# Kernel tuning notes

Hardware: AMD Instinct MI355X
Metric: run time of the kernel (lower is better)

The kernel has to match this reference:

```python
import jax, jax.numpy as jnp
import numpy as np

B, S, E = 4, 2048, 1024
H, D, F = 16, 64, 4096
EPS = 1e-5


def layer_norm(x, gamma, beta):
    mu = jnp.mean(x, axis=-1, keepdims=True)
    var = jnp.mean(jnp.square(x - mu), axis=-1, keepdims=True)
    return (x - mu) * jax.lax.rsqrt(var + EPS) * gamma + beta


def setup_inputs() -> dict:
    key = jax.random.key(0)
    ks = jax.random.split(key, 8)
    scale = 0.02  # keep logits in a numerically sane range
    X = jax.random.normal(ks[0], (B, S, E), dtype=jnp.float32)
    WQ = jax.random.normal(ks[1], (H, E, D), dtype=jnp.float32) * scale
    WK = jax.random.normal(ks[2], (H, E, D), dtype=jnp.float32) * scale
    WV = jax.random.normal(ks[3], (H, E, D), dtype=jnp.float32) * scale
    WO = jax.random.normal(ks[4], (H * D, E), dtype=jnp.float32) * scale
    gamma = jnp.ones((E,), dtype=jnp.float32)
    beta = jnp.zeros((E,), dtype=jnp.float32)
    W1 = jax.random.normal(ks[5], (E, F), dtype=jnp.float32) * scale
    b1 = jnp.zeros((F,), dtype=jnp.float32)
    W2 = jax.random.normal(ks[6], (F, E), dtype=jnp.float32) * scale
    b2 = jnp.zeros((E,), dtype=jnp.float32)
    return {"X": X, "WQ": WQ, "WK": WK, "WV": WV, "WO": WO,
            "gamma": gamma, "beta": beta, "W1": W1, "b1": b1, "W2": W2, "b2": b2}


def reference(X, WQ, WK, WV, WO, gamma, beta, W1, b1, W2, b2):
    # Batched-over-heads version of the per-head python loop (same math).
    Q = jnp.einsum('bse,hed->bhsd', X, WQ)  # [B,H,S,D]
    K = jnp.einsum('bse,hed->bhsd', X, WK)
    V = jnp.einsum('bse,hed->bhsd', X, WV)
    scores = jnp.einsum('bhsd,bhtd->bhst', Q, K)  # [B,H,S,T]
    # FAITHFUL quirk: torch.softmax(..., dim=1) on a [B,S,S] tensor normalizes
    # over the QUERY axis (axis=2 here), then divides by sqrt(D) AFTER softmax.
    att = jax.nn.softmax(scores, axis=2) / jnp.sqrt(jnp.float32(D))
    vec = jnp.einsum('bhst,bhtd->bhsd', att, V)  # [B,H,S,D]
    att_vec = jnp.transpose(vec, (0, 2, 1, 3)).reshape(X.shape[0], X.shape[1], H * D)
    vector_att = layer_norm(att_vec @ WO + X, gamma, beta)
    vector_ffn = jax.nn.relu(vector_att @ W1 + b1) @ W2 + b2
    return layer_norm(vector_ffn + vector_att, gamma, beta)
```

## Files before the change

### kernel.cpp

```cpp
#include <hip/hip_runtime.h>
#include <cstddef>
#include <cstdint>

#define BB 4
#define SS 2048
#define EE 1024
#define HH 16
#define DD 64
#define FF 4096

typedef unsigned short u16;
typedef __attribute__((ext_vector_type(8))) short short8;
typedef __attribute__((ext_vector_type(4))) short short4v;
typedef __attribute__((ext_vector_type(4))) float f32x4;

__device__ __forceinline__ u16 f2bf(float x) {
    unsigned u = __builtin_bit_cast(unsigned, x);
    u += 0x7fffu + ((u >> 16) & 1u);
    return (u16)(u >> 16);
}
__device__ __forceinline__ float bf2f(u16 h) {
    unsigned u = ((unsigned)h) << 16;
    return __builtin_bit_cast(float, u);
}

#define GLD_LDS16(g, l)                                                     \
    __builtin_amdgcn_global_load_lds(                                       \
        (const __attribute__((address_space(1))) void*)(g),                 \
        (__attribute__((address_space(3))) void*)(l), 16, 0, 0)

__global__ __launch_bounds__(256) void cvt_bf(const float* __restrict__ in,
                                              u16* __restrict__ out, int n4) {
    const int i = blockIdx.x * 256 + threadIdx.x;
    if (i < n4) {
        float4 v = reinterpret_cast<const float4*>(in)[i];
        short4v o;
        o.x = (short)f2bf(v.x); o.y = (short)f2bf(v.y);
        o.z = (short)f2bf(v.z); o.w = (short)f2bf(v.w);
        reinterpret_cast<short4v*>(out)[i] = o;
    }
}

__global__ __launch_bounds__(256) void transp_bf(const float* __restrict__ in,
                                                 u16* __restrict__ out, int R, int C) {
    __shared__ float T[64][65];
    const int r0 = blockIdx.x * 64, c0 = blockIdx.y * 64;
    const size_t zoff = (size_t)blockIdx.z * R * C;
    in += zoff; out += zoff;
    const int tid = threadIdx.x;
#pragma unroll 4
    for (int i = 0; i < 16; ++i) {
        int l = tid + i * 256;
        T[l >> 6][l & 63] = in[(size_t)(r0 + (l >> 6)) * C + c0 + (l & 63)];
    }
    __syncthreads();
#pragma unroll 4
    for (int i = 0; i < 16; ++i) {
        int l = tid + i * 256;
        out[(size_t)(c0 + (l >> 6)) * R + r0 + (l & 63)] = f2bf(T[l & 63][l >> 6]);
    }
}

template <int EPI>
__global__ __launch_bounds__(256) void gemm_bf16(const u16* __restrict__ A,
                                                 const u16* __restrict__ BT,
                                                 int K, int N,
                                                 void* __restrict__ Cout,
                                                 const float* __restrict__ bias,
                                                 const void* __restrict__ resid) {
    __shared__ u16 As[128 * 32];
    __shared__ u16 Bs[128 * 32];
    const int tid = threadIdx.x;
    const int w = tid >> 6, l = tid & 63;
    const int quad = l >> 4, lane16 = l & 15;
    const int wr = (w >> 1) * 64, wc = (w & 1) * 64;
    const int m0 = blockIdx.x * 128, n0 = blockIdx.y * 128;
    const int drow = w * 32 + (l >> 2);
    const int dk = (l & 3) * 8;
    const u16* Ag = A + (size_t)(m0 + drow) * K + dk;
    const u16* Bg = BT + (size_t)(n0 + drow) * K + dk;
    const size_t r16 = (size_t)16 * K;
    u16* AsD = &As[w * 1024];
    u16* BsD = &Bs[w * 1024];

    f32x4 acc[4][4] = {};
    for (int k0 = 0; k0 < K; k0 += 32) {
        __syncthreads();
        GLD_LDS16(Ag + k0, AsD);
        GLD_LDS16(Ag + k0 + r16, AsD + 512);
        GLD_LDS16(Bg + k0, BsD);
        GLD_LDS16(Bg + k0 + r16, BsD + 512);
        __syncthreads();
        short8 af[4], bf[4];
#pragma unroll
        for (int mf = 0; mf < 4; ++mf)
            af[mf] = *(const short8*)&As[(wr + mf * 16 + lane16) * 32 + quad * 8];
#pragma unroll
        for (int nf = 0; nf < 4; ++nf)
            bf[nf] = *(const short8*)&Bs[(wc + nf * 16 + lane16) * 32 + quad * 8];
#pragma unroll
        for (int mf = 0; mf < 4; ++mf)
#pragma unroll
            for (int nf = 0; nf < 4; ++nf)
                acc[mf][nf] = __builtin_amdgcn_mfma_f32_16x16x32_bf16(af[mf], bf[nf], acc[mf][nf], 0, 0, 0);
    }

#pragma unroll
    for (int mf = 0; mf < 4; ++mf) {
        const int row = m0 + wr + mf * 16 + quad * 4;
#pragma unroll
        for (int nf = 0; nf < 4; ++nf) {
            const int col = n0 + wc + nf * 16 + lane16;
#pragma unroll
            for (int r = 0; r < 4; ++r) {
                float v = acc[mf][nf][r];
                const size_t idx = (size_t)(row + r) * N + col;
                if (EPI == 0) {
                    ((u16*)Cout)[idx] = f2bf(v);
                } else if (EPI == 1) {
                    ((float*)Cout)[idx] = v + ((const float*)resid)[idx];
                } else if (EPI == 2) {
                    v += bias[col];
                    ((u16*)Cout)[idx] = f2bf(fmaxf(v, 0.f));
                } else {
                    v += bias[col] + bf2f(((const u16*)resid)[idx]);
                    ((float*)Cout)[idx] = v;
                }
            }
        }
    }
}

__global__ __launch_bounds__(256) void stats_l(const u16* __restrict__ Qg,
                                               const u16* __restrict__ Kg,
                                               float* __restrict__ Ls) {
    __shared__ u16 Qt[64 * 72];
    const int t0 = blockIdx.x * 128;
    const int bh = blockIdx.y;
    const int b = bh >> 4, h = bh & 15;
    const int tid = threadIdx.x;
    const int w = tid >> 6, l = tid & 63;
    const int quad = l >> 4, lane16 = l & 15;
    const u16* Qp = Qg + (size_t)b * SS * 1024 + h * 64;
    const u16* Kp = Kg + (size_t)b * SS * 1024 + h * 64;
    const int sr = tid >> 3;
    const int dg = (tid & 7) * 8;

    short8 kf[2][2];
#pragma unroll
    for (int nf = 0; nf < 2; ++nf)
#pragma unroll
        for (int ks = 0; ks < 2; ++ks)
            kf[nf][ks] = *(const short8*)(Kp +
                (size_t)(t0 + w * 32 + nf * 16 + lane16) * 1024 + ks * 32 + quad * 8);

    const u16* qsrc0 = Qp + (size_t)sr * 1024 + dg;
    short8 pq0 = *(const short8*)qsrc0;
    short8 pq1 = *(const short8*)(qsrc0 + (size_t)32 * 1024);

    float lcol[2] = {0.f, 0.f};
    for (int st = 0; st < 32; ++st) {
        __syncthreads();
        *(short8*)&Qt[sr * 72 + dg] = pq0;
        *(short8*)&Qt[(sr + 32) * 72 + dg] = pq1;
        __syncthreads();
        if (st + 1 < 32) {
            const u16* qsrc = Qp + (size_t)((st + 1) * 64 + sr) * 1024 + dg;
            pq0 = *(const short8*)qsrc;
            pq1 = *(const short8*)(qsrc + (size_t)32 * 1024);
        }
        f32x4 sc[4][2] = {};
#pragma unroll
        for (int ks = 0; ks < 2; ++ks) {
#pragma unroll
            for (int mf = 0; mf < 4; ++mf) {
                short8 afr = *(const short8*)&Qt[(mf * 16 + lane16) * 72 + ks * 32 + quad * 8];
#pragma unroll
                for (int nf = 0; nf < 2; ++nf)
                    sc[mf][nf] = __builtin_amdgcn_mfma_f32_16x16x32_bf16(afr, kf[nf][ks], sc[mf][nf], 0, 0, 0);
            }
        }
#pragma unroll
        for (int nf = 0; nf < 2; ++nf)
#pragma unroll
            for (int mf = 0; mf < 4; ++mf)
#pragma unroll
                for (int r = 0; r < 4; ++r) lcol[nf] += __expf(sc[mf][nf][r]);
    }
#pragma unroll
    for (int nf = 0; nf < 2; ++nf) {
        lcol[nf] += __shfl_xor(lcol[nf], 32);
        lcol[nf] += __shfl_xor(lcol[nf], 16);
        if (quad == 0)
            Ls[(size_t)bh * SS + t0 + w * 32 + nf * 16 + lane16] = lcol[nf];
    }
}

__global__ __launch_bounds__(256) void vscale(u16* __restrict__ Vtg,
                                              const float* __restrict__ Ls) {
    const int r = blockIdx.x;
    const int b = blockIdx.y;
    const int h = r >> 6;
    const int t0 = threadIdx.x * 8;
    u16* vp = Vtg + (size_t)r * 8192 + b * SS + t0;
    const float* lp = Ls + (size_t)(b * 16 + h) * SS + t0;
    short8 v = *(short8*)vp;
    short8 o;
#pragma unroll
    for (int i = 0; i < 8; ++i)
        o[i] = (short)f2bf(bf2f((u16)v[i]) * (0.125f / lp[i]));
    *(short8*)vp = o;
}

__global__ __launch_bounds__(256) void pv_fused(const u16* __restrict__ Qg,
                                                const u16* __restrict__ Kg,
                                                const u16* __restrict__ Vtg,
                                                u16* __restrict__ vecbf) {
    __shared__ u16 Ks[64 * 72];
    __shared__ u16 Vs[64 * 72];
    __shared__ u16 Ps[128 * 72];
    const int s0 = blockIdx.x * 128;
    const int bh = blockIdx.y;
    const int b = bh >> 4, h = bh & 15;
    const int tid = threadIdx.x;
    const int w = tid >> 6, l = tid & 63;
    const int quad = l >> 4, lane16 = l & 15;
    const u16* Qp = Qg + (size_t)b * SS * 1024 + h * 64;
    const u16* Kp = Kg + (size_t)b * SS * 1024 + h * 64;
    const u16* Vp = Vtg + (size_t)h * 64 * 8192 + (size_t)b * SS;
    const int sr = tid >> 3, dg = (tid & 7) * 8;

    short8 qf[2][2];
#pragma unroll
    for (int nf = 0; nf < 2; ++nf)
#pragma unroll
        for (int ks = 0; ks < 2; ++ks)
            qf[nf][ks] = *(const short8*)(Qp +
                (size_t)(s0 + w * 32 + nf * 16 + lane16) * 1024 + ks * 32 + quad * 8);

    short8 pk0 = *(const short8*)(Kp + (size_t)sr * 1024 + dg);
    short8 pk1 = *(const short8*)(Kp + (size_t)(sr + 32) * 1024 + dg);
    short8 pv0 = *(const short8*)(Vp + (size_t)sr * 8192 + dg);
    short8 pv1 = *(const short8*)(Vp + (size_t)(sr + 32) * 8192 + dg);

    f32x4 acc[2][4] = {};
    for (int tt = 0; tt < 32; ++tt) {
        __syncthreads();
        *(short8*)&Ks[sr * 72 + dg] = pk0;
        *(short8*)&Ks[(sr + 32) * 72 + dg] = pk1;
        *(short8*)&Vs[sr * 72 + dg] = pv0;
        *(short8*)&Vs[(sr + 32) * 72 + dg] = pv1;
        __syncthreads();
        if (tt + 1 < 32) {
            const int t1 = (tt + 1) * 64;
            pk0 = *(const short8*)(Kp + (size_t)(t1 + sr) * 1024 + dg);
            pk1 = *(const short8*)(Kp + (size_t)(t1 + sr + 32) * 1024 + dg);
            pv0 = *(const short8*)(Vp + (size_t)sr * 8192 + t1 + dg);
            pv1 = *(const short8*)(Vp + (size_t)(sr + 32) * 8192 + t1 + dg);
        }
        f32x4 sc[4][2] = {};
#pragma unroll
        for (int ks = 0; ks < 2; ++ks) {
#pragma unroll
            for (int mf = 0; mf < 4; ++mf) {
                short8 afr = *(const short8*)&Ks[(mf * 16 + lane16) * 72 + ks * 32 + quad * 8];
#pragma unroll
                for (int nf = 0; nf < 2; ++nf)
                    sc[mf][nf] = __builtin_amdgcn_mfma_f32_16x16x32_bf16(afr, qf[nf][ks], sc[mf][nf], 0, 0, 0);
            }
        }
#pragma unroll
        for (int mf = 0; mf < 4; ++mf)
#pragma unroll
            for (int nf = 0; nf < 2; ++nf) {
                const int srow = w * 32 + nf * 16 + lane16;
                short4v pk;
                pk.x = (short)f2bf(__expf(sc[mf][nf][0]));
                pk.y = (short)f2bf(__expf(sc[mf][nf][1]));
                pk.z = (short)f2bf(__expf(sc[mf][nf][2]));
                pk.w = (short)f2bf(__expf(sc[mf][nf][3]));
                *(short4v*)&Ps[srow * 72 + mf * 16 + quad * 4] = pk;
            }
#pragma unroll
        for (int ks = 0; ks < 2; ++ks) {
            short8 bfr[4];
#pragma unroll
            for (int nf = 0; nf < 4; ++nf)
                bfr[nf] = *(const short8*)&Vs[(nf * 16 + lane16) * 72 + ks * 32 + quad * 8];
            short8 afr[2];
#pragma unroll
            for (int mf = 0; mf < 2; ++mf)
                afr[mf] = *(const short8*)&Ps[(w * 32 + mf * 16 + lane16) * 72 + ks * 32 + quad * 8];
#pragma unroll
            for (int mf = 0; mf < 2; ++mf)
#pragma unroll
                for (int nf = 0; nf < 4; ++nf)
                    acc[mf][nf] = __builtin_amdgcn_mfma_f32_16x16x32_bf16(afr[mf], bfr[nf], acc[mf][nf], 0, 0, 0);
        }
    }
#pragma unroll
    for (int mf = 0; mf < 2; ++mf)
#pragma unroll
        for (int nf = 0; nf < 4; ++nf) {
            const int col = h * 64 + nf * 16 + lane16;
#pragma unroll
            for (int r = 0; r < 4; ++r) {
                const int srow = s0 + w * 32 + mf * 16 + quad * 4 + r;
                vecbf[(size_t)(b * SS + srow) * 1024 + col] = f2bf(acc[mf][nf][r]);
            }
        }
}

__global__ __launch_bounds__(256) void ln_bf_kernel(const float* __restrict__ buf,
                                                    const float* __restrict__ g,
                                                    const float* __restrict__ be,
                                                    u16* __restrict__ outbf) {
    const int row = blockIdx.x;
    const int tid = threadIdx.x;
    const float* p = buf + (size_t)row * EE;
    float4 x = reinterpret_cast<const float4*>(p)[tid];
    float s = x.x + x.y + x.z + x.w;
    __shared__ float red[4];
#pragma unroll
    for (int o = 32; o > 0; o >>= 1) s += __shfl_down(s, o);
    const int wid = tid >> 6, lane = tid & 63;
    if (lane == 0) red[wid] = s;
    __syncthreads();
    const float mu = (red[0] + red[1] + red[2] + red[3]) * (1.0f / EE);
    __syncthreads();
    const float dx = x.x - mu, dy = x.y - mu, dz = x.z - mu, dw = x.w - mu;
    float v = dx * dx + dy * dy + dz * dz + dw * dw;
#pragma unroll
    for (int o = 32; o > 0; o >>= 1) v += __shfl_down(v, o);
    if (lane == 0) red[wid] = v;
    __syncthreads();
    const float var = (red[0] + red[1] + red[2] + red[3]) * (1.0f / EE);
    const float rs = rsqrtf(var + 1e-5f);
    float4 gv = reinterpret_cast<const float4*>(g)[tid];
    float4 bv = reinterpret_cast<const float4*>(be)[tid];
    short4v o;
    o.x = (short)f2bf(dx * rs * gv.x + bv.x);
    o.y = (short)f2bf(dy * rs * gv.y + bv.y);
    o.z = (short)f2bf(dz * rs * gv.z + bv.z);
    o.w = (short)f2bf(dw * rs * gv.w + bv.w);
    reinterpret_cast<short4v*>(outbf + (size_t)row * EE)[tid] = o;
}

__global__ __launch_bounds__(256) void ln_kernel(float* __restrict__ buf,
                                                 const float* __restrict__ g,
                                                 const float* __restrict__ be) {
    const int row = blockIdx.x;
    const int tid = threadIdx.x;
    float* p = buf + (size_t)row * EE;
    float4 x = reinterpret_cast<float4*>(p)[tid];
    float s = x.x + x.y + x.z + x.w;
    __shared__ float red[4];
#pragma unroll
    for (int o = 32; o > 0; o >>= 1) s += __shfl_down(s, o);
    const int wid = tid >> 6, lane = tid & 63;
    if (lane == 0) red[wid] = s;
    __syncthreads();
    const float mu = (red[0] + red[1] + red[2] + red[3]) * (1.0f / EE);
    __syncthreads();
    const float dx = x.x - mu, dy = x.y - mu, dz = x.z - mu, dw = x.w - mu;
    float v = dx * dx + dy * dy + dz * dz + dw * dw;
#pragma unroll
    for (int o = 32; o > 0; o >>= 1) v += __shfl_down(v, o);
    if (lane == 0) red[wid] = v;
    __syncthreads();
    const float var = (red[0] + red[1] + red[2] + red[3]) * (1.0f / EE);
    const float rs = rsqrtf(var + 1e-5f);
    float4 gv = reinterpret_cast<const float4*>(g)[tid];
    float4 bv = reinterpret_cast<const float4*>(be)[tid];
    float4 y;
    y.x = dx * rs * gv.x + bv.x;
    y.y = dy * rs * gv.y + bv.y;
    y.z = dz * rs * gv.z + bv.z;
    y.w = dw * rs * gv.w + bv.w;
    reinterpret_cast<float4*>(p)[tid] = y;
}

extern "C" void kernel_launch(void* const* d_in, const int* in_sizes, int n_in,
                              void* d_out, int out_size, void* d_ws, size_t ws_size,
                              hipStream_t stream) {
    const float* X     = (const float*)d_in[0];
    const float* WQ    = (const float*)d_in[1];
    const float* WK    = (const float*)d_in[2];
    const float* WV    = (const float*)d_in[3];
    const float* WO    = (const float*)d_in[4];
    const float* gamma = (const float*)d_in[5];
    const float* beta  = (const float*)d_in[6];
    const float* W1    = (const float*)d_in[7];
    const float* b1    = (const float*)d_in[8];
    const float* W2    = (const float*)d_in[9];
    const float* b2    = (const float*)d_in[10];
    float* out = (float*)d_out;

    char* ws = (char*)d_ws;
    const size_t MB = 1024 * 1024;
    u16* WQT   = (u16*)(ws + 0);
    u16* WKT   = (u16*)(ws + 2 * MB);
    u16* WVT   = (u16*)(ws + 4 * MB);
    u16* WOT   = (u16*)(ws + 6 * MB);
    u16* W1T   = (u16*)(ws + 8 * MB);
    u16* W2T   = (u16*)(ws + 16 * MB);
    float* Ls  = (float*)(ws + 24 * MB);
    u16* Qbf   = (u16*)(ws + 25 * MB);
    u16* Kbf   = (u16*)(ws + 41 * MB);
    u16* Vt    = (u16*)(ws + 57 * MB);
    u16* vecbf = (u16*)(ws + 73 * MB);
    u16* hid   = (u16*)(ws + 25 * MB);
    u16* Xbf   = (u16*)(ws + 89 * MB);
    float* vatt  = (float*)(ws + 105 * MB);
    u16*   ln1bf = (u16*)(ws + 137 * MB);

    const int NT = BB * SS;

    cvt_bf<<<8192, 256, 0, stream>>>(X, Xbf, NT * EE / 4);
    transp_bf<<<dim3(16, 1, 16), 256, 0, stream>>>(WQ, WQT, EE, DD);
    transp_bf<<<dim3(16, 1, 16), 256, 0, stream>>>(WK, WKT, EE, DD);
    transp_bf<<<dim3(16, 1, 16), 256, 0, stream>>>(WV, WVT, EE, DD);
    transp_bf<<<dim3(16, 16, 1), 256, 0, stream>>>(WO, WOT, HH * DD, EE);
    transp_bf<<<dim3(16, 64, 1), 256, 0, stream>>>(W1, W1T, EE, FF);
    transp_bf<<<dim3(64, 16, 1), 256, 0, stream>>>(W2, W2T, FF, EE);

    gemm_bf16<0><<<dim3(64, 8), 256, 0, stream>>>(Xbf, WQT, EE, 1024, Qbf, nullptr, nullptr);
    gemm_bf16<0><<<dim3(64, 8), 256, 0, stream>>>(Xbf, WKT, EE, 1024, Kbf, nullptr, nullptr);
    gemm_bf16<0><<<dim3(8, 64), 256, 0, stream>>>(WVT, Xbf, EE, 8192, Vt, nullptr, nullptr);

    stats_l<<<dim3(SS / 128, BB * HH), 256, 0, stream>>>(Qbf, Kbf, Ls);
    vscale<<<dim3(1024, BB), 256, 0, stream>>>(Vt, Ls);
    pv_fused<<<dim3(SS / 128, BB * HH), 256, 0, stream>>>(Qbf, Kbf, Vt, vecbf);

    gemm_bf16<1><<<dim3(64, 8), 256, 0, stream>>>(vecbf, WOT, EE, 1024, vatt, nullptr, X);
    ln_bf_kernel<<<NT, 256, 0, stream>>>(vatt, gamma, beta, ln1bf);

    gemm_bf16<2><<<dim3(64, 32), 256, 0, stream>>>(ln1bf, W1T, EE, FF, hid, b1, nullptr);
    gemm_bf16<3><<<dim3(64, 8), 256, 0, stream>>>(hid, W2T, FF, 1024, out, b2, ln1bf);

    ln_kernel<<<NT, 256, 0, stream>>>(out, gamma, beta);
}
```

Baseline: 644.5 us.

## Keep P in registers with 32x32 MFMA and permlane swap in pv_fused

Rewrites the attention PV kernel to use 32x32x16 bf16 MFMAs so the exponentiated score tile can be repacked in registers with v_permlane32_swap instead of going through an LDS P buffer. K/V tiles switch to an XOR-swizzled unpadded LDS layout. Q is pre-scaled by log2(e) in the projection GEMM epilogue so raw v_exp_f32 (exp2) replaces __expf in both the stats and PV kernels. This removes LDS round-trips and a barrier-free store/load of P, at the cost of inline asm and a layout change that must stay consistent with the MFMA output mapping.

```diff
diff --git a/kernel.cpp b/kernel.cpp
--- a/kernel.cpp
+++ b/kernel.cpp
@@ -13,6 +13,8 @@
 typedef __attribute__((ext_vector_type(8))) short short8;
 typedef __attribute__((ext_vector_type(4))) short short4v;
 typedef __attribute__((ext_vector_type(4))) float f32x4;
+typedef __attribute__((ext_vector_type(16))) float f32x16;
+typedef __attribute__((ext_vector_type(4))) unsigned u32x4;
 
 __device__ __forceinline__ u16 f2bf(float x) {
     unsigned u = __builtin_bit_cast(unsigned, x);
@@ -22,6 +24,22 @@
 __device__ __forceinline__ float bf2f(u16 h) {
     unsigned u = ((unsigned)h) << 16;
     return __builtin_bit_cast(float, u);
+}
+__device__ __forceinline__ float ex2(float x) {
+    float r;
+    asm("v_exp_f32 %0, %1" : "=v"(r) : "v"(x));
+    return r;
+}
+__device__ __forceinline__ unsigned cvtpk(float lo, float hi) {
+    unsigned r;
+    asm("v_cvt_pk_bf16_f32 %0, %1, %2" : "=v"(r) : "v"(lo), "v"(hi));
+    return r;
+}
+__device__ __forceinline__ void pl32swap(unsigned &a, unsigned &b) {
+    asm("s_nop 1\n\tv_permlane32_swap_b32 %0, %1\n\ts_nop 1" : "+v"(a), "+v"(b));
+}
+__device__ __forceinline__ int sw(int row, int lbyte) {
+    return row * 128 + (lbyte ^ ((row & 7) << 4));
 }
 
 #define GLD_LDS16(g, l)                                                     \
@@ -67,7 +85,8 @@
                                                  int K, int N,
                                                  void* __restrict__ Cout,
                                                  const float* __restrict__ bias,
-                                                 const void* __restrict__ resid) {
+                                                 const void* __restrict__ resid,
+                                                 float oscale) {
     __shared__ u16 As[128 * 32];
     __shared__ u16 Bs[128 * 32];
     const int tid = threadIdx.x;
@@ -116,7 +135,7 @@
                 float v = acc[mf][nf][r];
                 const size_t idx = (size_t)(row + r) * N + col;
                 if (EPI == 0) {
-                    ((u16*)Cout)[idx] = f2bf(v);
+                    ((u16*)Cout)[idx] = f2bf(v * oscale);
                 } else if (EPI == 1) {
                     ((float*)Cout)[idx] = v + ((const float*)resid)[idx];
                 } else if (EPI == 2) {
@@ -185,7 +204,7 @@
 #pragma unroll
             for (int mf = 0; mf < 4; ++mf)
 #pragma unroll
-                for (int r = 0; r < 4; ++r) lcol[nf] += __expf(sc[mf][nf][r]);
+                for (int r = 0; r < 4; ++r) lcol[nf] += ex2(sc[mf][nf][r]);
     }
 #pragma unroll
     for (int nf = 0; nf < 2; ++nf) {
@@ -216,40 +235,36 @@
                                                 const u16* __restrict__ Kg,
                                                 const u16* __restrict__ Vtg,
                                                 u16* __restrict__ vecbf) {
-    __shared__ u16 Ks[64 * 72];
-    __shared__ u16 Vs[64 * 72];
-    __shared__ u16 Ps[128 * 72];
+    __shared__ u16 Ks[64 * 64];
+    __shared__ u16 Vs[64 * 64];
     const int s0 = blockIdx.x * 128;
     const int bh = blockIdx.y;
     const int b = bh >> 4, h = bh & 15;
     const int tid = threadIdx.x;
     const int w = tid >> 6, l = tid & 63;
-    const int quad = l >> 4, lane16 = l & 15;
+    const int l32 = l & 31, hf = l >> 5;
     const u16* Qp = Qg + (size_t)b * SS * 1024 + h * 64;
     const u16* Kp = Kg + (size_t)b * SS * 1024 + h * 64;
     const u16* Vp = Vtg + (size_t)h * 64 * 8192 + (size_t)b * SS;
     const int sr = tid >> 3, dg = (tid & 7) * 8;
 
-    short8 qf[2][2];
-#pragma unroll
-    for (int nf = 0; nf < 2; ++nf)
-#pragma unroll
-        for (int ks = 0; ks < 2; ++ks)
-            qf[nf][ks] = *(const short8*)(Qp +
-                (size_t)(s0 + w * 32 + nf * 16 + lane16) * 1024 + ks * 32 + quad * 8);
+    short8 qf[4];
+#pragma unroll
+    for (int ks = 0; ks < 4; ++ks)
+        qf[ks] = *(const short8*)(Qp + (size_t)(s0 + w * 32 + l32) * 1024 + ks * 16 + hf * 8);
 
     short8 pk0 = *(const short8*)(Kp + (size_t)sr * 1024 + dg);
     short8 pk1 = *(const short8*)(Kp + (size_t)(sr + 32) * 1024 + dg);
     short8 pv0 = *(const short8*)(Vp + (size_t)sr * 8192 + dg);
     short8 pv1 = *(const short8*)(Vp + (size_t)(sr + 32) * 8192 + dg);
 
-    f32x4 acc[2][4] = {};
+    f32x16 acc[2] = {};
     for (int tt = 0; tt < 32; ++tt) {
         __syncthreads();
-        *(short8*)&Ks[sr * 72 + dg] = pk0;
-        *(short8*)&Ks[(sr + 32) * 72 + dg] = pk1;
-        *(short8*)&Vs[sr * 72 + dg] = pv0;
-        *(short8*)&Vs[(sr + 32) * 72 + dg] = pv1;
+        *(short8*)((char*)Ks + sw(sr, dg * 2)) = pk0;
+        *(short8*)((char*)Ks + sw(sr + 32, dg * 2)) = pk1;
+        *(short8*)((char*)Vs + sw(sr, dg * 2)) = pv0;
+        *(short8*)((char*)Vs + sw(sr + 32, dg * 2)) = pv1;
         __syncthreads();
         if (tt + 1 < 32) {
             const int t1 = (tt + 1) * 64;
@@ -258,57 +273,49 @@
             pv0 = *(const short8*)(Vp + (size_t)sr * 8192 + t1 + dg);
             pv1 = *(const short8*)(Vp + (size_t)(sr + 32) * 8192 + t1 + dg);
         }
-        f32x4 sc[4][2] = {};
-#pragma unroll
-        for (int ks = 0; ks < 2; ++ks) {
-#pragma unroll
-            for (int mf = 0; mf < 4; ++mf) {
-                short8 afr = *(const short8*)&Ks[(mf * 16 + lane16) * 72 + ks * 32 + quad * 8];
-#pragma unroll
-                for (int nf = 0; nf < 2; ++nf)
-                    sc[mf][nf] = __builtin_amdgcn_mfma_f32_16x16x32_bf16(afr, qf[nf][ks], sc[mf][nf], 0, 0, 0);
+        f32x16 sc0 = {}, sc1 = {};
+#pragma unroll
+        for (int ks = 0; ks < 4; ++ks) {
+            short8 a0 = *(const short8*)((char*)Ks + sw(l32, ks * 32 + hf * 16));
+            short8 a1 = *(const short8*)((char*)Ks + sw(32 + l32, ks * 32 + hf * 16));
+            sc0 = __builtin_amdgcn_mfma_f32_32x32x16_bf16(a0, qf[ks], sc0, 0, 0, 0);
+            sc1 = __builtin_amdgcn_mfma_f32_32x32x16_bf16(a1, qf[ks], sc1, 0, 0, 0);
+        }
+        unsigned cp0[8], cp1[8];
+#pragma unroll
+        for (int p = 0; p < 8; ++p) {
+            cp0[p] = cvtpk(ex2(sc0[2 * p]), ex2(sc0[2 * p + 1]));
+            cp1[p] = cvtpk(ex2(sc1[2 * p]), ex2(sc1[2 * p + 1]));
+        }
+        short8 pa[4];
+#pragma unroll
+        for (int ks2 = 0; ks2 < 4; ++ks2) {
+            unsigned* cp = (ks2 & 2) ? cp1 : cp0;
+            const int c = (ks2 & 1) * 4;
+            unsigned w0 = cp[c + 0], w2 = cp[c + 2];
+            unsigned w1 = cp[c + 1], w3 = cp[c + 3];
+            pl32swap(w0, w2);
+            pl32swap(w1, w3);
+            u32x4 t4; t4.x = w0; t4.y = w1; t4.z = w2; t4.w = w3;
+            pa[ks2] = __builtin_bit_cast(short8, t4);
+        }
+#pragma unroll
+        for (int ks2 = 0; ks2 < 4; ++ks2)
+#pragma unroll
+            for (int nf = 0; nf < 2; ++nf) {
+                short8 bfr = *(const short8*)((char*)Vs + sw(nf * 32 + l32, ks2 * 32 + hf * 16));
+                acc[nf] = __builtin_amdgcn_mfma_f32_32x32x16_bf16(pa[ks2], bfr, acc[nf], 0, 0, 0);
             }
-        }
-#pragma unroll
-        for (int mf = 0; mf < 4; ++mf)
-#pragma unroll
-            for (int nf = 0; nf < 2; ++nf) {
-                const int srow = w * 32 + nf * 16 + lane16;
-                short4v pk;
-                pk.x = (short)f2bf(__expf(sc[mf][nf][0]));
-                pk.y = (short)f2bf(__expf(sc[mf][nf][1]));
-                pk.z = (short)f2bf(__expf(sc[mf][nf][2]));
-                pk.w = (short)f2bf(__expf(sc[mf][nf][3]));
-                *(short4v*)&Ps[srow * 72 + mf * 16 + quad * 4] = pk;
-            }
-#pragma unroll
-        for (int ks = 0; ks < 2; ++ks) {
-            short8 bfr[4];
-#pragma unroll
-            for (int nf = 0; nf < 4; ++nf)
-                bfr[nf] = *(const short8*)&Vs[(nf * 16 + lane16) * 72 + ks * 32 + quad * 8];
-            short8 afr[2];
-#pragma unroll
-            for (int mf = 0; mf < 2; ++mf)
-                afr[mf] = *(const short8*)&Ps[(w * 32 + mf * 16 + lane16) * 72 + ks * 32 + quad * 8];
-#pragma unroll
-            for (int mf = 0; mf < 2; ++mf)
-#pragma unroll
-                for (int nf = 0; nf < 4; ++nf)
-                    acc[mf][nf] = __builtin_amdgcn_mfma_f32_16x16x32_bf16(afr[mf], bfr[nf], acc[mf][nf], 0, 0, 0);
-        }
-    }
-#pragma unroll
-    for (int mf = 0; mf < 2; ++mf)
-#pragma unroll
-        for (int nf = 0; nf < 4; ++nf) {
-            const int col = h * 64 + nf * 16 + lane16;
-#pragma unroll
-            for (int r = 0; r < 4; ++r) {
-                const int srow = s0 + w * 32 + mf * 16 + quad * 4 + r;
-                vecbf[(size_t)(b * SS + srow) * 1024 + col] = f2bf(acc[mf][nf][r]);
-            }
-        }
+    }
+#pragma unroll
+    for (int nf = 0; nf < 2; ++nf) {
+        const int col = h * 64 + nf * 32 + l32;
+#pragma unroll
+        for (int r = 0; r < 16; ++r) {
+            const int srow = s0 + w * 32 + (r & 3) + 8 * (r >> 2) + 4 * hf;
+            vecbf[(size_t)(b * SS + srow) * 1024 + col] = f2bf(acc[nf][r]);
+        }
+    }
 }
 
 __global__ __launch_bounds__(256) void ln_bf_kernel(const float* __restrict__ buf,
@@ -424,19 +431,19 @@
     transp_bf<<<dim3(16, 64, 1), 256, 0, stream>>>(W1, W1T, EE, FF);
     transp_bf<<<dim3(64, 16, 1), 256, 0, stream>>>(W2, W2T, FF, EE);
 
-    gemm_bf16<0><<<dim3(64, 8), 256, 0, stream>>>(Xbf, WQT, EE, 1024, Qbf, nullptr, nullptr);
-    gemm_bf16<0><<<dim3(64, 8), 256, 0, stream>>>(Xbf, WKT, EE, 1024, Kbf, nullptr, nullptr);
-    gemm_bf16<0><<<dim3(8, 64), 256, 0, stream>>>(WVT, Xbf, EE, 8192, Vt, nullptr, nullptr);
+    gemm_bf16<0><<<dim3(64, 8), 256, 0, stream>>>(Xbf, WQT, EE, 1024, Qbf, nullptr, nullptr, 1.44269504089f);
+    gemm_bf16<0><<<dim3(64, 8), 256, 0, stream>>>(Xbf, WKT, EE, 1024, Kbf, nullptr, nullptr, 1.0f);
+    gemm_bf16<0><<<dim3(8, 64), 256, 0, stream>>>(WVT, Xbf, EE, 8192, Vt, nullptr, nullptr, 1.0f);
 
     stats_l<<<dim3(SS / 128, BB * HH), 256, 0, stream>>>(Qbf, Kbf, Ls);
     vscale<<<dim3(1024, BB), 256, 0, stream>>>(Vt, Ls);
     pv_fused<<<dim3(SS / 128, BB * HH), 256, 0, stream>>>(Qbf, Kbf, Vt, vecbf);
 
-    gemm_bf16<1><<<dim3(64, 8), 256, 0, stream>>>(vecbf, WOT, EE, 1024, vatt, nullptr, X);
+    gemm_bf16<1><<<dim3(64, 8), 256, 0, stream>>>(vecbf, WOT, EE, 1024, vatt, nullptr, X, 1.0f);
     ln_bf_kernel<<<NT, 256, 0, stream>>>(vatt, gamma, beta, ln1bf);
 
-    gemm_bf16<2><<<dim3(64, 32), 256, 0, stream>>>(ln1bf, W1T, EE, FF, hid, b1, nullptr);
-    gemm_bf16<3><<<dim3(64, 8), 256, 0, stream>>>(hid, W2T, FF, 1024, out, b2, ln1bf);
+    gemm_bf16<2><<<dim3(64, 32), 256, 0, stream>>>(ln1bf, W1T, EE, FF, hid, b1, nullptr, 1.0f);
+    gemm_bf16<3><<<dim3(64, 8), 256, 0, stream>>>(hid, W2T, FF, 1024, out, b2, ln1bf, 1.0f);
 
     ln_kernel<<<NT, 256, 0, stream>>>(out, gamma, beta);
 }
```

Result: faster. 630.7 us (-2.1%).
